# Kernel tuning notes

Measured on AMD Instinct MI355X. Metric: run time of the kernel, lower is better.

## Reference

```python
import jax, jax.numpy as jnp
import numpy as np

B, S, Q, C = 1, 128, 256, 256
H, DH = 8, 32
TOT = H * DH  # 256


def setup_inputs() -> dict:
    key = jax.random.key(0)
    ks = jax.random.split(key, 12)
    inp = {
        'q_x': jax.random.normal(ks[0], (B, S, Q, C), jnp.float32),
        'kv_x': jax.random.normal(ks[1], (B, S, Q, C), jnp.float32),
        'bias_mask': jax.random.normal(ks[2], (B, S, 1, 1, Q), jnp.float32),
        'bias_pair': jax.random.normal(ks[3], (B, 1, H, Q, Q), jnp.float32),
        # torch nn.Linear weights are (out_features, in_features)
        'Wq': jax.random.normal(ks[4], (TOT, C), jnp.float32) * (C ** -0.5),
        'Wk': jax.random.normal(ks[5], (TOT, C), jnp.float32) * (C ** -0.5),
        'Wv': jax.random.normal(ks[6], (TOT, C), jnp.float32) * (C ** -0.5),
        'Wg': jax.random.normal(ks[7], (TOT, C), jnp.float32) * 0.02,
        'bg': jnp.ones((TOT,), jnp.float32),   # 'gating' init: zero W, bias=1
        'Wo': jax.random.normal(ks[8], (C, TOT), jnp.float32) * 0.02,
        'bo': jnp.zeros((C,), jnp.float32),
    }
    return inp


def reference(q_x, kv_x, bias_mask, bias_pair, Wq, Wk, Wv, Wg, bg, Wo, bo):
    # QKV projections (no bias), split heads, move head dim before Q: [B,S,H,Q,DH]
    def proj(x, W):
        y = jnp.einsum('bsqc,dc->bsqd', x, W)
        return y.reshape(*y.shape[:-1], H, DH).transpose(0, 1, 3, 2, 4)

    q = proj(q_x, Wq)   # NOTE: literal source applies NO 1/sqrt(dh) scaling in naive mode
    k = proj(kv_x, Wk)
    v = proj(kv_x, Wv)

    # scores [B,S,H,Q,K] with additive biases, manual softmax
    scores = jnp.einsum('bshqd,bshkd->bshqk', q, k) + bias_mask + bias_pair
    a = jax.nn.softmax(scores, axis=-1)
    o = jnp.einsum('bshqk,bshkd->bshqd', a, v)
    o = o.transpose(0, 1, 3, 2, 4)  # [B,S,Q,H,DH]

    # gating
    g = jax.nn.sigmoid(jnp.einsum('bsqc,dc->bsqd', q_x, Wg) + bg)
    o = o * g.reshape(*g.shape[:-1], H, DH)

    # output projection
    o = o.reshape(*o.shape[:-2], TOT)
    return jnp.einsum('bsqd,cd->bsqc', o, Wo) + bo
```

## Files before the change

kernel.cpp:

```cpp
#include <hip/hip_runtime.h>


typedef unsigned short u16;
typedef unsigned int   u32;
typedef float  f32x4  __attribute__((ext_vector_type(4)));
typedef __bf16 bf16x8 __attribute__((ext_vector_type(8)));

__device__ __forceinline__ float bf2f(u16 u) {
    union { u32 i; float f; } v; v.i = ((u32)u) << 16; return v.f;
}
__device__ __forceinline__ u16 f2bf(float f) {
    __bf16 h = (__bf16)f; return __builtin_bit_cast(u16, h);
}

__device__ __forceinline__ void gld16(const u16* g, u16* l) {
    __builtin_amdgcn_global_load_lds(
        (const __attribute__((address_space(1))) u32*)g,
        (__attribute__((address_space(3))) u32*)l, 16, 0, 0);
}

__device__ __forceinline__ size_t hm(int row, int col) {
    const int s = row >> 8, q = row & 255, h = col >> 5, dh = col & 31;
    return ((size_t)((h * 128 + s) * 256 + q) << 5) + dh;
}

__device__ __forceinline__ void cvt8(const float4* src, u16* dst) {
    float4 a = src[0], b = src[1];
    u16 r[8];
    r[0] = f2bf(a.x); r[1] = f2bf(a.y); r[2] = f2bf(a.z); r[3] = f2bf(a.w);
    r[4] = f2bf(b.x); r[5] = f2bf(b.y); r[6] = f2bf(b.z); r[7] = f2bf(b.w);
    *(uint4*)dst = *(uint4*)r;
}

__global__ __launch_bounds__(256) void prep(
    const float* __restrict__ qx, const float* __restrict__ kvx,
    const float* __restrict__ Wq, const float* __restrict__ Wk,
    const float* __restrict__ Wv, const float* __restrict__ Wg,
    const float* __restrict__ Wo, const float* __restrict__ bp,
    u16* __restrict__ Xq, u16* __restrict__ Xkv, u16* __restrict__ Wball,
    float* __restrict__ bppf)
{
    const int b = blockIdx.x, t = threadIdx.x;
    if (b < 4096) {
        const int e = (b * 256 + t) * 8;
        cvt8((const float4*)(qx + e), Xq + e);
    } else if (b < 8192) {
        const int e = ((b - 4096) * 256 + t) * 8;
        cvt8((const float4*)(kvx + e), Xkv + e);
    } else if (b < 8352) {
        const int b2  = b - 8192;
        const int mat = b2 >> 5;
        const float* W = (mat == 0) ? Wq : (mat == 1) ? Wk : (mat == 2) ? Wv
                       : (mat == 3) ? Wg : Wo;
        const int off = (b2 & 31) * 2048 + t * 8;
        cvt8((const float4*)(W + off), Wball + mat * 65536 + off);
    } else {
        const int b3 = b - 8352;
        const int u0 = (b3 * 256 + t) * 2;
        #pragma unroll
        for (int k2 = 0; k2 < 2; ++k2) {
            const int u  = u0 + k2;
            const int l  = u & 63;
            const int nt = (u >> 6) & 15;
            const int tt = u >> 10;
            const int ww = tt & 3, qqt = (tt >> 2) & 3, hh = tt >> 4;
            const int qb = qqt * 64 + ww * 16 + (l >> 4) * 4;
            const int kp = nt * 16 + (l & 15);
            const float* src = bp + (size_t)(hh * 256 + qb) * 256 + kp;
            float4 v;
            v.x = src[0]; v.y = src[256]; v.z = src[512]; v.w = src[768];
            *(float4*)(bppf + (size_t)u * 4) = v;
        }
    }
}

__global__ __launch_bounds__(256) void proj_all(
    const u16* __restrict__ Xq, const u16* __restrict__ Xkv,
    const u16* __restrict__ Wball, const float* __restrict__ bg,
    u16* __restrict__ Qh, u16* __restrict__ Kh, u16* __restrict__ Vh, u16* __restrict__ Gh)
{
    __shared__ u16 At[128 * 64];
    __shared__ u16 Wt[128 * 64];

    const int bid = blockIdx.x;
    const int mb  = bid & 255;
    const int nb  = bid >> 8;
    const int t   = nb >> 1;
    const int n0  = (nb & 1) * 128;
    const int m0  = mb * 128;
    const u16* A = (t == 0 || t == 3) ? Xq : Xkv;
    const u16* W = Wball + t * 65536;
    u16*       O = (t == 0) ? Qh : (t == 1) ? Kh : (t == 2) ? Vh : Gh;

    const int tid  = threadIdx.x;
    const int lane = tid & 63;
    const int w    = tid >> 6;
    const int quad = lane >> 4;
    const int ln   = lane & 15;
    const int wm   = (w >> 1) * 64;
    const int wn   = (w & 1) * 64;
    const int lrow = lane >> 3;
    const int lcol = (lane & 7) * 8;

    f32x4 acc[4][4] = {};

    for (int k0 = 0; k0 < 256; k0 += 64) {
        __syncthreads();
        #pragma unroll
        for (int qq = 0; qq < 4; ++qq) {
            const int r = w * 32 + qq * 8;
            gld16(A + (size_t)(m0 + r + lrow) * 256 + k0 + lcol, &At[r * 64]);
            gld16(W + (size_t)(n0 + r + lrow) * 256 + k0 + lcol, &Wt[r * 64]);
        }
        __syncthreads();

        #pragma unroll
        for (int kk = 0; kk < 2; ++kk) {
            const int kc = kk * 32 + quad * 8;
            bf16x8 af[4], bfr[4];
            #pragma unroll
            for (int i = 0; i < 4; ++i)
                af[i] = __builtin_bit_cast(bf16x8, *(const uint4*)&At[(wm + i * 16 + ln) * 64 + kc]);
            #pragma unroll
            for (int j = 0; j < 4; ++j)
                bfr[j] = __builtin_bit_cast(bf16x8, *(const uint4*)&Wt[(wn + j * 16 + ln) * 64 + kc]);
            #pragma unroll
            for (int i = 0; i < 4; ++i)
                #pragma unroll
                for (int j = 0; j < 4; ++j)
                    acc[i][j] = __builtin_amdgcn_mfma_f32_16x16x32_bf16(bfr[j], af[i], acc[i][j], 0, 0, 0);
        }
    }

    const int act = (t == 3);
    #pragma unroll
    for (int i = 0; i < 4; ++i) {
        const int row = m0 + wm + i * 16 + ln;
        #pragma unroll
        for (int j = 0; j < 4; ++j) {
            const int colb = n0 + wn + j * 16 + quad * 4;
            u16 r4[4];
            if (act) {
                const float4 bgv = *(const float4*)&bg[colb];
                float v0 = acc[i][j][0] + bgv.x;
                float v1 = acc[i][j][1] + bgv.y;
                float v2 = acc[i][j][2] + bgv.z;
                float v3 = acc[i][j][3] + bgv.w;
                r4[0] = f2bf(1.0f / (1.0f + __expf(-v0)));
                r4[1] = f2bf(1.0f / (1.0f + __expf(-v1)));
                r4[2] = f2bf(1.0f / (1.0f + __expf(-v2)));
                r4[3] = f2bf(1.0f / (1.0f + __expf(-v3)));
            } else {
                r4[0] = f2bf(acc[i][j][0]);
                r4[1] = f2bf(acc[i][j][1]);
                r4[2] = f2bf(acc[i][j][2]);
                r4[3] = f2bf(acc[i][j][3]);
            }
            *(uint2*)(O + hm(row, colb)) = *(const uint2*)r4;
        }
    }
}

__global__ __launch_bounds__(256) void gemm_out(
    const u16* __restrict__ Oh, const u16* __restrict__ Wob,
    const float* __restrict__ bo, float* __restrict__ out)
{
    __shared__ u16 At[64 * 64];
    __shared__ u16 Wt[128 * 64];

    const int bid = blockIdx.x;
    const int m0  = (bid & 511) * 64;
    const int n0  = (bid >> 9) * 128;

    const int tid  = threadIdx.x;
    const int lane = tid & 63;
    const int w    = tid >> 6;
    const int quad = lane >> 4;
    const int ln   = lane & 15;
    const int wm   = (w >> 1) * 32;
    const int wn   = (w & 1) * 64;
    const int lrow = lane >> 3;
    const int lcol = (lane & 7) * 8;

    f32x4 acc[2][4] = {};

    for (int k0 = 0; k0 < 256; k0 += 64) {
        __syncthreads();
        #pragma unroll
        for (int qq = 0; qq < 2; ++qq) {
            const int r = w * 16 + qq * 8;
            gld16(Oh + hm(m0 + r + lrow, k0 + lcol), &At[r * 64]);
        }
        #pragma unroll
        for (int qq = 0; qq < 4; ++qq) {
            const int r = w * 32 + qq * 8;
            gld16(Wob + (size_t)(n0 + r + lrow) * 256 + k0 + lcol, &Wt[r * 64]);
        }
        __syncthreads();

        #pragma unroll
        for (int kk = 0; kk < 2; ++kk) {
            const int kc = kk * 32 + quad * 8;
            bf16x8 af[2], bfr[4];
            #pragma unroll
            for (int i = 0; i < 2; ++i)
                af[i] = __builtin_bit_cast(bf16x8, *(const uint4*)&At[(wm + i * 16 + ln) * 64 + kc]);
            #pragma unroll
            for (int j = 0; j < 4; ++j)
                bfr[j] = __builtin_bit_cast(bf16x8, *(const uint4*)&Wt[(wn + j * 16 + ln) * 64 + kc]);
            #pragma unroll
            for (int i = 0; i < 2; ++i)
                #pragma unroll
                for (int j = 0; j < 4; ++j)
                    acc[i][j] = __builtin_amdgcn_mfma_f32_16x16x32_bf16(bfr[j], af[i], acc[i][j], 0, 0, 0);
        }
    }

    #pragma unroll
    for (int i = 0; i < 2; ++i) {
        const int row = m0 + wm + i * 16 + ln;
        #pragma unroll
        for (int j = 0; j < 4; ++j) {
            const int colb = n0 + wn + j * 16 + quad * 4;
            const float4 bov = *(const float4*)&bo[colb];
            float4 o;
            o.x = acc[i][j][0] + bov.x;
            o.y = acc[i][j][1] + bov.y;
            o.z = acc[i][j][2] + bov.z;
            o.w = acc[i][j][3] + bov.w;
            *(float4*)&out[(size_t)row * 256 + colb] = o;
        }
    }
}

__global__ __launch_bounds__(256, 2) void attn_kernel(
    const u16* __restrict__ Qh, const u16* __restrict__ Kh, const u16* __restrict__ Vh,
    const u16* __restrict__ Gh, const float* __restrict__ bm, const float* __restrict__ bppf,
    u16* __restrict__ Oh)
{
    __shared__ u16   Vt[32][264];
    __shared__ u16   Pl[4][16][76];
    __shared__ float bmf[256];

    const int hs   = blockIdx.x;
    const int h    = hs & 7;
    const int s    = hs >> 3;
    const int tid  = threadIdx.x;
    const int lane = tid & 63;
    const int w    = tid >> 6;
    const int quad = lane >> 4;
    const int ln   = lane & 15;

    const size_t hsBase = ((size_t)(h * 128 + s) * 256) << 5;

    {
        const uint4* vp = (const uint4*)(Vh + hsBase + (size_t)tid * 32);
        uint4 vv0 = vp[0], vv1 = vp[1], vv2 = vp[2], vv3 = vp[3];
        u16 tmp[32];
        *(uint4*)&tmp[0]  = vv0; *(uint4*)&tmp[8]  = vv1;
        *(uint4*)&tmp[16] = vv2; *(uint4*)&tmp[24] = vv3;
        #pragma unroll
        for (int dh = 0; dh < 32; ++dh) Vt[dh][tid] = tmp[dh];
        bmf[tid] = bm[s * 256 + tid];
    }
    __syncthreads();

    for (int iq = 0; iq < 2; ++iq) {
        const int qt = blockIdx.y * 2 + iq;
        const int q0 = qt * 64 + w * 16;

        bf16x8 aq = __builtin_bit_cast(bf16x8,
            *(const uint4*)(Qh + hsBase + (size_t)(q0 + ln) * 32 + quad * 8));

        f32x4 sc[16];
        #pragma unroll
        for (int nt = 0; nt < 16; ++nt) {
            bf16x8 bk = __builtin_bit_cast(bf16x8,
                *(const uint4*)(Kh + hsBase + (size_t)(nt * 16 + ln) * 32 + quad * 8));
            f32x4 z = {0.f, 0.f, 0.f, 0.f};
            sc[nt] = __builtin_amdgcn_mfma_f32_16x16x32_bf16(aq, bk, z, 0, 0, 0);
        }

        const float* bpt = bppf + ((size_t)(((h * 4 + qt) * 4 + w) * 16) * 64 + lane) * 4;
        float rmax[4] = {-1e30f, -1e30f, -1e30f, -1e30f};
        #pragma unroll
        for (int nt = 0; nt < 16; ++nt) {
            const f32x4 bv = *(const f32x4*)(bpt + (size_t)nt * 256);
            const float bmv = bmf[nt * 16 + ln];
            #pragma unroll
            for (int rr = 0; rr < 4; ++rr) {
                float v = sc[nt][rr] + bmv + bv[rr];
                sc[nt][rr] = v;
                rmax[rr] = fmaxf(rmax[rr], v);
            }
        }
        #pragma unroll
        for (int rr = 0; rr < 4; ++rr) {
            float m = rmax[rr];
            m = fmaxf(m, __shfl_xor(m, 1));
            m = fmaxf(m, __shfl_xor(m, 2));
            m = fmaxf(m, __shfl_xor(m, 4));
            m = fmaxf(m, __shfl_xor(m, 8));
            rmax[rr] = m;
        }
        float rsum[4] = {0.f, 0.f, 0.f, 0.f};
        #pragma unroll
        for (int nt = 0; nt < 16; ++nt)
            #pragma unroll
            for (int rr = 0; rr < 4; ++rr) {
                float p = __expf(sc[nt][rr] - rmax[rr]);
                sc[nt][rr] = p;
                rsum[rr] += p;
            }
        float rinv[4];
        #pragma unroll
        for (int rr = 0; rr < 4; ++rr) {
            float t = rsum[rr];
            t += __shfl_xor(t, 1);
            t += __shfl_xor(t, 2);
            t += __shfl_xor(t, 4);
            t += __shfl_xor(t, 8);
            rinv[rr] = 1.0f / t;
        }

        f32x4 o0 = {0.f, 0.f, 0.f, 0.f}, o1 = {0.f, 0.f, 0.f, 0.f};
        #pragma unroll
        for (int c = 0; c < 4; ++c) {
            #pragma unroll
            for (int ntl = 0; ntl < 4; ++ntl) {
                const int nt = c * 4 + ntl;
                #pragma unroll
                for (int rr = 0; rr < 4; ++rr)
                    Pl[w][quad * 4 + rr][ntl * 16 + ln] = f2bf(sc[nt][rr] * rinv[rr]);
            }
            #pragma unroll
            for (int kcl = 0; kcl < 2; ++kcl) {
                bf16x8 pa = __builtin_bit_cast(bf16x8, *(const uint4*)&Pl[w][ln][kcl * 32 + quad * 8]);
                bf16x8 v0 = __builtin_bit_cast(bf16x8, *(const uint4*)&Vt[ln][c * 64 + kcl * 32 + quad * 8]);
                bf16x8 v1 = __builtin_bit_cast(bf16x8, *(const uint4*)&Vt[16 + ln][c * 64 + kcl * 32 + quad * 8]);
                o0 = __builtin_amdgcn_mfma_f32_16x16x32_bf16(pa, v0, o0, 0, 0, 0);
                o1 = __builtin_amdgcn_mfma_f32_16x16x32_bf16(pa, v1, o1, 0, 0, 0);
            }
        }

        #pragma unroll
        for (int rr = 0; rr < 4; ++rr) {
            const int q = q0 + quad * 4 + rr;
            const size_t base = hsBase + (size_t)q * 32;
            float g0 = bf2f(Gh[base + ln]);
            float g1 = bf2f(Gh[base + 16 + ln]);
            Oh[base + ln]      = f2bf(o0[rr] * g0);
            Oh[base + 16 + ln] = f2bf(o1[rr] * g1);
        }
    }
}

extern "C" void kernel_launch(void* const* d_in, const int* in_sizes, int n_in,
                              void* d_out, int out_size, void* d_ws, size_t ws_size,
                              hipStream_t stream)
{
    const float* qx  = (const float*)d_in[0];
    const float* kvx = (const float*)d_in[1];
    const float* bm  = (const float*)d_in[2];
    const float* bp  = (const float*)d_in[3];
    const float* Wq  = (const float*)d_in[4];
    const float* Wk  = (const float*)d_in[5];
    const float* Wv  = (const float*)d_in[6];
    const float* Wg  = (const float*)d_in[7];
    const float* bg  = (const float*)d_in[8];
    const float* Wo  = (const float*)d_in[9];
    const float* bo  = (const float*)d_in[10];
    float* out = (float*)d_out;

    const size_t NEL = (size_t)32768 * 256;
    u16* Qh = (u16*)d_ws;
    u16* Kh = Qh + NEL;
    u16* Vh = Kh + NEL;
    u16* Gh = Vh + NEL;
    u16* Wball = Gh + NEL;
    float* bppf = (float*)(Wball + 5 * 65536);

    u16* Xq  = (u16*)d_out;
    u16* Xkv = Xq + NEL;

    prep<<<dim3(8608), dim3(256), 0, stream>>>(qx, kvx, Wq, Wk, Wv, Wg, Wo, bp,
                                               Xq, Xkv, Wball, bppf);

    proj_all<<<dim3(2048), dim3(256), 0, stream>>>(Xq, Xkv, Wball, bg, Qh, Kh, Vh, Gh);

    attn_kernel<<<dim3(1024, 2), dim3(256), 0, stream>>>(Qh, Kh, Vh, Gh, bm, bppf, Qh );

    gemm_out<<<dim3(1024), dim3(256), 0, stream>>>(Qh , Wball + 4 * 65536, bo, out);
}
```

Before: 221.0 us.

## Transpose attention MFMA outputs so each lane holds a query row's keys

Swaps the A/B operands of the QK^T and PV MFMAs so the accumulator is transposed, with each lane owning one query row and four consecutive keys. Row max and sum then need only two cross-lane shuffles per row instead of four shuffles for each of four rows. Bias, P, gate and output accesses become packed vector loads and stores, and the bias_pair prepack switches to float4 reads to match the new layout. The risk is that the prepack ordering and the attention kernel indexing must agree exactly, and the change touches several interacting parts.

```diff
diff --git a/kernel.cpp b/kernel.cpp
--- a/kernel.cpp
+++ b/kernel.cpp
@@ -64,11 +64,9 @@
             const int nt = (u >> 6) & 15;
             const int tt = u >> 10;
             const int ww = tt & 3, qqt = (tt >> 2) & 3, hh = tt >> 4;
-            const int qb = qqt * 64 + ww * 16 + (l >> 4) * 4;
-            const int kp = nt * 16 + (l & 15);
-            const float* src = bp + (size_t)(hh * 256 + qb) * 256 + kp;
-            float4 v;
-            v.x = src[0]; v.y = src[256]; v.z = src[512]; v.w = src[768];
+            const int q  = qqt * 64 + ww * 16 + (l & 15);
+            const int kp = nt * 16 + (l >> 4) * 4;
+            const float4 v = *(const float4*)(bp + (size_t)(hh * 256 + q) * 256 + kp);
             *(float4*)(bppf + (size_t)u * 4) = v;
         }
     }
@@ -278,50 +276,39 @@
             bf16x8 bk = __builtin_bit_cast(bf16x8,
                 *(const uint4*)(Kh + hsBase + (size_t)(nt * 16 + ln) * 32 + quad * 8));
             f32x4 z = {0.f, 0.f, 0.f, 0.f};
-            sc[nt] = __builtin_amdgcn_mfma_f32_16x16x32_bf16(aq, bk, z, 0, 0, 0);
+            sc[nt] = __builtin_amdgcn_mfma_f32_16x16x32_bf16(bk, aq, z, 0, 0, 0);
         }
 
         const float* bpt = bppf + ((size_t)(((h * 4 + qt) * 4 + w) * 16) * 64 + lane) * 4;
         float rmax[4] = {-1e30f, -1e30f, -1e30f, -1e30f};
         #pragma unroll
         for (int nt = 0; nt < 16; ++nt) {
-            const f32x4 bv = *(const f32x4*)(bpt + (size_t)nt * 256);
-            const float bmv = bmf[nt * 16 + ln];
+            const f32x4 bv  = *(const f32x4*)(bpt + (size_t)nt * 256);
+            const f32x4 bm4 = *(const f32x4*)&bmf[nt * 16 + quad * 4];
             #pragma unroll
             for (int rr = 0; rr < 4; ++rr) {
-                float v = sc[nt][rr] + bmv + bv[rr];
+                float v = sc[nt][rr] + bm4[rr] + bv[rr];
                 sc[nt][rr] = v;
                 rmax[rr] = fmaxf(rmax[rr], v);
             }
         }
-        #pragma unroll
-        for (int rr = 0; rr < 4; ++rr) {
-            float m = rmax[rr];
-            m = fmaxf(m, __shfl_xor(m, 1));
-            m = fmaxf(m, __shfl_xor(m, 2));
-            m = fmaxf(m, __shfl_xor(m, 4));
-            m = fmaxf(m, __shfl_xor(m, 8));
-            rmax[rr] = m;
-        }
-        float rsum[4] = {0.f, 0.f, 0.f, 0.f};
+        float m = fmaxf(fmaxf(rmax[0], rmax[1]), fmaxf(rmax[2], rmax[3]));
+        m = fmaxf(m, __shfl_xor(m, 16));
+        m = fmaxf(m, __shfl_xor(m, 32));
+
+        float s4[4] = {0.f, 0.f, 0.f, 0.f};
         #pragma unroll
         for (int nt = 0; nt < 16; ++nt)
             #pragma unroll
             for (int rr = 0; rr < 4; ++rr) {
-                float p = __expf(sc[nt][rr] - rmax[rr]);
+                float p = __expf(sc[nt][rr] - m);
                 sc[nt][rr] = p;
-                rsum[rr] += p;
-            }
-        float rinv[4];
-        #pragma unroll
-        for (int rr = 0; rr < 4; ++rr) {
-            float t = rsum[rr];
-            t += __shfl_xor(t, 1);
-            t += __shfl_xor(t, 2);
-            t += __shfl_xor(t, 4);
-            t += __shfl_xor(t, 8);
-            rinv[rr] = 1.0f / t;
-        }
+                s4[rr] += p;
+            }
+        float tsum = (s4[0] + s4[1]) + (s4[2] + s4[3]);
+        tsum += __shfl_xor(tsum, 16);
+        tsum += __shfl_xor(tsum, 32);
+        const float rinv = 1.0f / tsum;
 
         f32x4 o0 = {0.f, 0.f, 0.f, 0.f}, o1 = {0.f, 0.f, 0.f, 0.f};
         #pragma unroll
@@ -329,29 +316,35 @@
             #pragma unroll
             for (int ntl = 0; ntl < 4; ++ntl) {
                 const int nt = c * 4 + ntl;
+                u16 r4[4];
                 #pragma unroll
                 for (int rr = 0; rr < 4; ++rr)
-                    Pl[w][quad * 4 + rr][ntl * 16 + ln] = f2bf(sc[nt][rr] * rinv[rr]);
+                    r4[rr] = f2bf(sc[nt][rr] * rinv);
+                *(uint2*)&Pl[w][ln][ntl * 16 + quad * 4] = *(const uint2*)r4;
             }
             #pragma unroll
             for (int kcl = 0; kcl < 2; ++kcl) {
                 bf16x8 pa = __builtin_bit_cast(bf16x8, *(const uint4*)&Pl[w][ln][kcl * 32 + quad * 8]);
                 bf16x8 v0 = __builtin_bit_cast(bf16x8, *(const uint4*)&Vt[ln][c * 64 + kcl * 32 + quad * 8]);
                 bf16x8 v1 = __builtin_bit_cast(bf16x8, *(const uint4*)&Vt[16 + ln][c * 64 + kcl * 32 + quad * 8]);
-                o0 = __builtin_amdgcn_mfma_f32_16x16x32_bf16(pa, v0, o0, 0, 0, 0);
-                o1 = __builtin_amdgcn_mfma_f32_16x16x32_bf16(pa, v1, o1, 0, 0, 0);
-            }
-        }
-
+                o0 = __builtin_amdgcn_mfma_f32_16x16x32_bf16(v0, pa, o0, 0, 0, 0);
+                o1 = __builtin_amdgcn_mfma_f32_16x16x32_bf16(v1, pa, o1, 0, 0, 0);
+            }
+        }
+
+        const size_t base = hsBase + (size_t)(q0 + ln) * 32;
+        const uint2 ga = *(const uint2*)(Gh + base + quad * 4);
+        const uint2 gb = *(const uint2*)(Gh + base + 16 + quad * 4);
+        const u16* gau = (const u16*)&ga;
+        const u16* gbu = (const u16*)&gb;
+        u16 ra[4], rb[4];
         #pragma unroll
         for (int rr = 0; rr < 4; ++rr) {
-            const int q = q0 + quad * 4 + rr;
-            const size_t base = hsBase + (size_t)q * 32;
-            float g0 = bf2f(Gh[base + ln]);
-            float g1 = bf2f(Gh[base + 16 + ln]);
-            Oh[base + ln]      = f2bf(o0[rr] * g0);
-            Oh[base + 16 + ln] = f2bf(o1[rr] * g1);
-        }
+            ra[rr] = f2bf(o0[rr] * bf2f(gau[rr]));
+            rb[rr] = f2bf(o1[rr] * bf2f(gbu[rr]));
+        }
+        *(uint2*)(Oh + base + quad * 4)      = *(const uint2*)ra;
+        *(uint2*)(Oh + base + 16 + quad * 4) = *(const uint2*)rb;
     }
 }
 
```

Result: slower. 251.0 us (+13.6%).
